# Performance work log

Hardware: AMD Instinct MI355X
Metric: run time of the kernel (lower is better)

## Reference

```python
import jax, jax.numpy as jnp
import numpy as np

N = 50000
E = 800000
F = 64
OUT = 64
K = 3


def setup_inputs() -> dict:
    key = jax.random.key(0)
    k1, k2, k3, k4, k5, k6 = jax.random.split(key, 6)
    x = jax.random.normal(k1, (N, F), dtype=jnp.float32)
    edge_row = jax.random.randint(k2, (E,), 0, N, dtype=jnp.int32)
    edge_col = jax.random.randint(k3, (E,), 0, N, dtype=jnp.int32)
    # positive edge weights (e.g., normalized adjacency values)
    edge_val = jax.random.uniform(k4, (E,), dtype=jnp.float32)
    W = jax.random.normal(k5, (F * (K + 1), OUT), dtype=jnp.float32) / np.sqrt(F * (K + 1))
    b = jax.random.normal(k6, (OUT,), dtype=jnp.float32) * 0.01
    return {"x": x, "edge_row": edge_row, "edge_col": edge_col,
            "edge_val": edge_val, "W": W, "b": b}


def _spmm(edge_row, edge_col, edge_val, h, n):
    # row i of adj @ h : sum over edges (i, j, v) of v * h[j]
    return jax.ops.segment_sum(edge_val[:, None] * h[edge_col], edge_row,
                               num_segments=n)


def reference(x, edge_row, edge_col, edge_val, W, b):
    out = x
    xs = [x]
    for _ in range(K):
        out = _spmm(edge_row, edge_col, edge_val, out, N)
        xs.append(out)
    h = jnp.concatenate(xs, axis=-1)  # [N, F*(K+1)]
    return h @ W + b
```

## Files before the change

### kernel.cpp

```cpp
#include <hip/hip_runtime.h>


#define F 64
#define OUT 64
#define SCAN_ELEMS 1024
#define NPART 8
#define CB_SHIFT 13

__global__ __launch_bounds__(256) void zero_buf(int4* __restrict__ p, int n4) {
  int i = blockIdx.x * 256 + threadIdx.x;
  if (i < n4) p[i] = make_int4(0, 0, 0, 0);
}

__global__ __launch_bounds__(256) void count_part(
    const int* __restrict__ row, const int* __restrict__ col,
    int* __restrict__ counts, int E, int rpp, int ncb) {
  int part = blockIdx.x & (NPART - 1);
  int e = (blockIdx.x >> 3) * 256 + threadIdx.x;
  if (e >= E) return;
  int r = __builtin_nontemporal_load(&row[e]);
  if ((unsigned)(r - part * rpp) >= (unsigned)rpp) return;
  int c = __builtin_nontemporal_load(&col[e]);
  atomicAdd(&counts[r * ncb + (c >> CB_SHIFT)], 1);
}

__global__ __launch_bounds__(256) void block_scan(
    const int* __restrict__ counts, int* __restrict__ offsets,
    int* __restrict__ blockSums, int B) {
  __shared__ int s[256];
  int t = threadIdx.x;
  int base = blockIdx.x * SCAN_ELEMS + t * 4;
  int v0 = 0, v1 = 0, v2 = 0, v3 = 0;
  if (base + 3 < B) {
    int4 c = *(const int4*)&counts[base];
    v0 = c.x; v1 = c.y; v2 = c.z; v3 = c.w;
  } else {
    if (base < B)     v0 = counts[base];
    if (base + 1 < B) v1 = counts[base + 1];
    if (base + 2 < B) v2 = counts[base + 2];
  }
  s[t] = v0 + v1 + v2 + v3;
  __syncthreads();
  for (int d = 1; d < 256; d <<= 1) {
    int x = (t >= d) ? s[t - d] : 0;
    __syncthreads();
    s[t] += x;
    __syncthreads();
  }
  int ex = (t == 0) ? 0 : s[t - 1];
  if (t == 255) blockSums[blockIdx.x] = s[255];
  int o0 = ex, o1 = o0 + v0, o2 = o1 + v1, o3 = o2 + v2;
  if (base + 3 < B) {
    *(int4*)&offsets[base] = make_int4(o0, o1, o2, o3);
  } else {
    if (base < B)     offsets[base]     = o0;
    if (base + 1 < B) offsets[base + 1] = o1;
    if (base + 2 < B) offsets[base + 2] = o2;
  }
}

__global__ __launch_bounds__(64) void scan_sums(int* __restrict__ bs, int nb) {
  int lane = threadIdx.x;
  int chunk = (nb + 63) / 64;
  int b = lane * chunk, e = min(b + chunk, nb);
  int sum = 0;
  for (int i = b; i < e; ++i) sum += bs[i];
  int incl = sum;
  for (int d = 1; d < 64; d <<= 1) {
    int u = __shfl_up(incl, d, 64);
    if (lane >= d) incl += u;
  }
  int run = incl - sum;
  for (int i = b; i < e; ++i) { int c = bs[i]; bs[i] = run; run += c; }
}

__global__ __launch_bounds__(256) void add_offsets(
    int* __restrict__ offsets, const int* __restrict__ blockSums,
    int* __restrict__ cursor, int B, int E) {
  int i = blockIdx.x * 256 + threadIdx.x;
  if (i < B) {
    int o = offsets[i] + blockSums[i >> 10];
    offsets[i] = o;
    cursor[i] = o;
  }
  if (i == 0) offsets[B] = E;
}

__global__ __launch_bounds__(256) void scatter_part(
    const int* __restrict__ row, const int* __restrict__ col,
    const float* __restrict__ val, int* __restrict__ cursor,
    float2* __restrict__ recs, int E, int rpp, int ncb) {
  int part = blockIdx.x & (NPART - 1);
  int e = (blockIdx.x >> 3) * 256 + threadIdx.x;
  if (e >= E) return;
  int r = __builtin_nontemporal_load(&row[e]);
  if ((unsigned)(r - part * rpp) >= (unsigned)rpp) return;
  int c = __builtin_nontemporal_load(&col[e]);
  float v = __builtin_nontemporal_load(&val[e]);
  int p = atomicAdd(&cursor[r * ncb + (c >> CB_SHIFT)], 1);
  recs[p] = make_float2(__int_as_float(c), v);
}

__global__ __launch_bounds__(256) void spmm_g16(
    const int* __restrict__ off, const float2* __restrict__ recs,
    const float* __restrict__ hin, float* __restrict__ hout, int N, int ncb) {
  int r = (blockIdx.x * 256 + threadIdx.x) >> 4;
  if (r >= N) return;
  int fp = (threadIdx.x & 15) << 2;
  int i = off[r * ncb], end = off[r * ncb + ncb];
  float4 acc = make_float4(0.f, 0.f, 0.f, 0.f);

  for (; i + 4 <= end; i += 4) {
    float2 e0 = recs[i], e1 = recs[i + 1], e2 = recs[i + 2], e3 = recs[i + 3];
    float4 h0 = *(const float4*)&hin[(size_t)__float_as_int(e0.x) * F + fp];
    float4 h1 = *(const float4*)&hin[(size_t)__float_as_int(e1.x) * F + fp];
    float4 h2 = *(const float4*)&hin[(size_t)__float_as_int(e2.x) * F + fp];
    float4 h3 = *(const float4*)&hin[(size_t)__float_as_int(e3.x) * F + fp];
    acc.x = fmaf(e0.y, h0.x, acc.x); acc.y = fmaf(e0.y, h0.y, acc.y);
    acc.z = fmaf(e0.y, h0.z, acc.z); acc.w = fmaf(e0.y, h0.w, acc.w);
    acc.x = fmaf(e1.y, h1.x, acc.x); acc.y = fmaf(e1.y, h1.y, acc.y);
    acc.z = fmaf(e1.y, h1.z, acc.z); acc.w = fmaf(e1.y, h1.w, acc.w);
    acc.x = fmaf(e2.y, h2.x, acc.x); acc.y = fmaf(e2.y, h2.y, acc.y);
    acc.z = fmaf(e2.y, h2.z, acc.z); acc.w = fmaf(e2.y, h2.w, acc.w);
    acc.x = fmaf(e3.y, h3.x, acc.x); acc.y = fmaf(e3.y, h3.y, acc.y);
    acc.z = fmaf(e3.y, h3.z, acc.z); acc.w = fmaf(e3.y, h3.w, acc.w);
  }
  for (; i < end; ++i) {
    float2 e0 = recs[i];
    float4 h0 = *(const float4*)&hin[(size_t)__float_as_int(e0.x) * F + fp];
    acc.x = fmaf(e0.y, h0.x, acc.x); acc.y = fmaf(e0.y, h0.y, acc.y);
    acc.z = fmaf(e0.y, h0.z, acc.z); acc.w = fmaf(e0.y, h0.w, acc.w);
  }
  *(float4*)&hout[(size_t)r * F + fp] = acc;
}

__global__ __launch_bounds__(256) void gemm_fused4_v5(
    const float* __restrict__ h0, const float* __restrict__ h1,
    const float* __restrict__ h2, const float* __restrict__ W,
    const float* __restrict__ bias, float* __restrict__ out, int N) {
  __shared__ float Ws[64 * 64];
  const float* hs[4] = {h0, h1, h2, out};

  int t = threadIdx.x;
  int oq = t & 3;
  int og = oq << 4;
  int ns = t >> 2;
  int node0 = blockIdx.x * 128;
  int n0 = min(node0 + ns, N - 1);
  int n1 = min(node0 + ns + 64, N - 1);

  const float4* b4 = (const float4*)bias;
  float4 acc[2][4];
#pragma unroll
  for (int m = 0; m < 4; ++m) { acc[0][m] = b4[oq * 4 + m]; acc[1][m] = acc[0][m]; }

#pragma unroll
  for (int s = 0; s < 4; ++s) {
    __syncthreads();
    const float4* Wg = (const float4*)(W + s * 4096);
#pragma unroll
    for (int i = 0; i < 4; ++i) ((float4*)Ws)[t + i * 256] = Wg[t + i * 256];
    __syncthreads();

    const float4* hr0 = (const float4*)(hs[s] + (size_t)n0 * F);
    const float4* hr1 = (const float4*)(hs[s] + (size_t)n1 * F);
    float4 hc0 = hr0[0], hc1 = hr1[0], hn0, hn1;

#pragma unroll 2
    for (int k4 = 0; k4 < 16; ++k4) {
      if (k4 < 15) { hn0 = hr0[k4 + 1]; hn1 = hr1[k4 + 1]; }
#pragma unroll
      for (int j = 0; j < 4; ++j) {
        const float4* w4 = (const float4*)&Ws[(k4 * 4 + j) * 64 + og];
        float4 w0 = w4[0], w1 = w4[1], w2 = w4[2], w3 = w4[3];
        float a = (j == 0) ? hc0.x : (j == 1) ? hc0.y : (j == 2) ? hc0.z : hc0.w;
        float c = (j == 0) ? hc1.x : (j == 1) ? hc1.y : (j == 2) ? hc1.z : hc1.w;
        acc[0][0].x = fmaf(a, w0.x, acc[0][0].x); acc[0][0].y = fmaf(a, w0.y, acc[0][0].y);
        acc[0][0].z = fmaf(a, w0.z, acc[0][0].z); acc[0][0].w = fmaf(a, w0.w, acc[0][0].w);
        acc[0][1].x = fmaf(a, w1.x, acc[0][1].x); acc[0][1].y = fmaf(a, w1.y, acc[0][1].y);
        acc[0][1].z = fmaf(a, w1.z, acc[0][1].z); acc[0][1].w = fmaf(a, w1.w, acc[0][1].w);
        acc[0][2].x = fmaf(a, w2.x, acc[0][2].x); acc[0][2].y = fmaf(a, w2.y, acc[0][2].y);
        acc[0][2].z = fmaf(a, w2.z, acc[0][2].z); acc[0][2].w = fmaf(a, w2.w, acc[0][2].w);
        acc[0][3].x = fmaf(a, w3.x, acc[0][3].x); acc[0][3].y = fmaf(a, w3.y, acc[0][3].y);
        acc[0][3].z = fmaf(a, w3.z, acc[0][3].z); acc[0][3].w = fmaf(a, w3.w, acc[0][3].w);
        acc[1][0].x = fmaf(c, w0.x, acc[1][0].x); acc[1][0].y = fmaf(c, w0.y, acc[1][0].y);
        acc[1][0].z = fmaf(c, w0.z, acc[1][0].z); acc[1][0].w = fmaf(c, w0.w, acc[1][0].w);
        acc[1][1].x = fmaf(c, w1.x, acc[1][1].x); acc[1][1].y = fmaf(c, w1.y, acc[1][1].y);
        acc[1][1].z = fmaf(c, w1.z, acc[1][1].z); acc[1][1].w = fmaf(c, w1.w, acc[1][1].w);
        acc[1][2].x = fmaf(c, w2.x, acc[1][2].x); acc[1][2].y = fmaf(c, w2.y, acc[1][2].y);
        acc[1][2].z = fmaf(c, w2.z, acc[1][2].z); acc[1][2].w = fmaf(c, w2.w, acc[1][2].w);
        acc[1][3].x = fmaf(c, w3.x, acc[1][3].x); acc[1][3].y = fmaf(c, w3.y, acc[1][3].y);
        acc[1][3].z = fmaf(c, w3.z, acc[1][3].z); acc[1][3].w = fmaf(c, w3.w, acc[1][3].w);
      }
      if (k4 < 15) { hc0 = hn0; hc1 = hn1; }
    }
  }

  int m0 = node0 + ns, m1 = node0 + ns + 64;
  if (m0 < N) {
    float4* o4 = (float4*)&out[(size_t)m0 * OUT + og];
    o4[0] = acc[0][0]; o4[1] = acc[0][1]; o4[2] = acc[0][2]; o4[3] = acc[0][3];
  }
  if (m1 < N) {
    float4* o4 = (float4*)&out[(size_t)m1 * OUT + og];
    o4[0] = acc[1][0]; o4[1] = acc[1][1]; o4[2] = acc[1][2]; o4[3] = acc[1][3];
  }
}

extern "C" void kernel_launch(void* const* d_in, const int* in_sizes, int n_in,
                              void* d_out, int out_size, void* d_ws, size_t ws_size,
                              hipStream_t stream) {
  const float* x    = (const float*)d_in[0];
  const int*   erow = (const int*)d_in[1];
  const int*   ecol = (const int*)d_in[2];
  const float* eval = (const float*)d_in[3];
  const float* W    = (const float*)d_in[4];
  const float* b    = (const float*)d_in[5];
  float* out = (float*)d_out;

  int N = in_sizes[0] / F;
  int E = in_sizes[1];
  size_t SZ = (size_t)N * F * sizeof(float);
  int ncb = ((N - 1) >> CB_SHIFT) + 1;
  int B = N * ncb;
  int nScanBlocks = (B + SCAN_ELEMS - 1) / SCAN_ELEMS;
  int rpp = (N + NPART - 1) / NPART;

  char* p = (char*)d_ws;
  float*  hA     = (float*)p;  p += SZ;
  float*  hB     = (float*)p;  p += SZ;
  float2* recs   = (float2*)p; p += (size_t)E * sizeof(float2);
  int*    counts = (int*)p;    p += (((size_t)B + 3) & ~3ull) * sizeof(int);
  int*    offs   = (int*)p;    p += (size_t)(B + 1) * sizeof(int);
  int*    cursor = (int*)p;    p += (size_t)B * sizeof(int);
  int*    bsums  = (int*)p;    p += (size_t)nScanBlocks * sizeof(int);

  int egrid = (E + 255) / 256;
  int g16grid = ((size_t)N * 16 + 255) / 256;
  int ggrid = (N + 127) / 128;
  int n4 = (B + 3) / 4;

  zero_buf<<<(n4 + 255) / 256, 256, 0, stream>>>((int4*)counts, n4);
  count_part<<<egrid * NPART, 256, 0, stream>>>(erow, ecol, counts, E, rpp, ncb);
  block_scan<<<nScanBlocks, 256, 0, stream>>>(counts, offs, bsums, B);
  scan_sums<<<1, 64, 0, stream>>>(bsums, nScanBlocks);
  add_offsets<<<(B + 255) / 256, 256, 0, stream>>>(offs, bsums, cursor, B, E);
  scatter_part<<<egrid * NPART, 256, 0, stream>>>(erow, ecol, eval, cursor, recs, E, rpp, ncb);

  spmm_g16<<<g16grid, 256, 0, stream>>>(offs, recs, x, hA, N, ncb);
  spmm_g16<<<g16grid, 256, 0, stream>>>(offs, recs, hA, hB, N, ncb);
  spmm_g16<<<g16grid, 256, 0, stream>>>(offs, recs, hB, out, N, ncb);

  gemm_fused4_v5<<<ggrid, 256, 0, stream>>>(x, hA, hB, W, b, out, N);
}
```

Baseline: 207.5 us.

## Project features through W first, then apply SpMM via Horner scheme

The four 64x64 slices of W are now applied to x up front (x·W0+b, x·W1, x·W2, x·W3), and the propagation becomes a Horner-style chain: yB += A·yC, yA += A·yB, out += A·yA. This drops the final GEMM kernel's dependency on the propagated features, so the dense projection can run in the same launch as the edge scatter. The scatter and the projection are merged into one kernel whose blocks branch on blockIdx to overlap the two. It costs one extra N×64 workspace buffer, an extra read of the addend in each SpMM, and a different floating-point summation order.

```diff
diff --git a/kernel.cpp b/kernel.cpp
--- a/kernel.cpp
+++ b/kernel.cpp
@@ -86,36 +86,113 @@
   if (i == 0) offsets[B] = E;
 }
 
-__global__ __launch_bounds__(256) void scatter_part(
+__global__ __launch_bounds__(256) void phaseB(
+    const float* __restrict__ x, const float* __restrict__ W,
+    const float* __restrict__ bias, float* __restrict__ out,
+    float* __restrict__ yA, float* __restrict__ yB, float* __restrict__ yC,
     const int* __restrict__ row, const int* __restrict__ col,
     const float* __restrict__ val, int* __restrict__ cursor,
-    float2* __restrict__ recs, int E, int rpp, int ncb) {
-  int part = blockIdx.x & (NPART - 1);
-  int e = (blockIdx.x >> 3) * 256 + threadIdx.x;
-  if (e >= E) return;
-  int r = __builtin_nontemporal_load(&row[e]);
-  if ((unsigned)(r - part * rpp) >= (unsigned)rpp) return;
-  int c = __builtin_nontemporal_load(&col[e]);
-  float v = __builtin_nontemporal_load(&val[e]);
-  int p = atomicAdd(&cursor[r * ncb + (c >> CB_SHIFT)], 1);
-  recs[p] = make_float2(__int_as_float(c), v);
-}
-
-__global__ __launch_bounds__(256) void spmm_g16(
+    float2* __restrict__ recs, int E, int rpp, int ncb, int N, int ggrid) {
+  if ((int)blockIdx.x < ggrid) {
+    __shared__ float Ws[4096];
+    float* dsts[4] = {out, yA, yB, yC};
+    int t = threadIdx.x;
+    int oq = t & 3;
+    int og = oq << 4;
+    int ns = t >> 2;
+    int node0 = blockIdx.x * 128;
+    int n0 = min(node0 + ns, N - 1);
+    int n1 = min(node0 + ns + 64, N - 1);
+    const float4* b4 = (const float4*)bias;
+    const float4* hr0 = (const float4*)(x + (size_t)n0 * F);
+    const float4* hr1 = (const float4*)(x + (size_t)n1 * F);
+
+#pragma unroll
+    for (int s = 0; s < 4; ++s) {
+      __syncthreads();
+      const float4* Wg = (const float4*)(W + s * 4096);
+#pragma unroll
+      for (int i = 0; i < 4; ++i) ((float4*)Ws)[t + i * 256] = Wg[t + i * 256];
+      __syncthreads();
+
+      float4 a0[4], a1[4];
+#pragma unroll
+      for (int m = 0; m < 4; ++m) {
+        a0[m] = (s == 0) ? b4[oq * 4 + m] : make_float4(0.f, 0.f, 0.f, 0.f);
+        a1[m] = a0[m];
+      }
+
+      float4 hc0 = hr0[0], hc1 = hr1[0], hn0, hn1;
+#pragma unroll 2
+      for (int k4 = 0; k4 < 16; ++k4) {
+        if (k4 < 15) { hn0 = hr0[k4 + 1]; hn1 = hr1[k4 + 1]; }
+#pragma unroll
+        for (int j = 0; j < 4; ++j) {
+          const float4* w4 = (const float4*)&Ws[(k4 * 4 + j) * 64 + og];
+          float4 w0 = w4[0], w1 = w4[1], w2 = w4[2], w3 = w4[3];
+          float a = (j == 0) ? hc0.x : (j == 1) ? hc0.y : (j == 2) ? hc0.z : hc0.w;
+          float c = (j == 0) ? hc1.x : (j == 1) ? hc1.y : (j == 2) ? hc1.z : hc1.w;
+          a0[0].x = fmaf(a, w0.x, a0[0].x); a0[0].y = fmaf(a, w0.y, a0[0].y);
+          a0[0].z = fmaf(a, w0.z, a0[0].z); a0[0].w = fmaf(a, w0.w, a0[0].w);
+          a0[1].x = fmaf(a, w1.x, a0[1].x); a0[1].y = fmaf(a, w1.y, a0[1].y);
+          a0[1].z = fmaf(a, w1.z, a0[1].z); a0[1].w = fmaf(a, w1.w, a0[1].w);
+          a0[2].x = fmaf(a, w2.x, a0[2].x); a0[2].y = fmaf(a, w2.y, a0[2].y);
+          a0[2].z = fmaf(a, w2.z, a0[2].z); a0[2].w = fmaf(a, w2.w, a0[2].w);
+          a0[3].x = fmaf(a, w3.x, a0[3].x); a0[3].y = fmaf(a, w3.y, a0[3].y);
+          a0[3].z = fmaf(a, w3.z, a0[3].z); a0[3].w = fmaf(a, w3.w, a0[3].w);
+          a1[0].x = fmaf(c, w0.x, a1[0].x); a1[0].y = fmaf(c, w0.y, a1[0].y);
+          a1[0].z = fmaf(c, w0.z, a1[0].z); a1[0].w = fmaf(c, w0.w, a1[0].w);
+          a1[1].x = fmaf(c, w1.x, a1[1].x); a1[1].y = fmaf(c, w1.y, a1[1].y);
+          a1[1].z = fmaf(c, w1.z, a1[1].z); a1[1].w = fmaf(c, w1.w, a1[1].w);
+          a1[2].x = fmaf(c, w2.x, a1[2].x); a1[2].y = fmaf(c, w2.y, a1[2].y);
+          a1[2].z = fmaf(c, w2.z, a1[2].z); a1[2].w = fmaf(c, w2.w, a1[2].w);
+          a1[3].x = fmaf(c, w3.x, a1[3].x); a1[3].y = fmaf(c, w3.y, a1[3].y);
+          a1[3].z = fmaf(c, w3.z, a1[3].z); a1[3].w = fmaf(c, w3.w, a1[3].w);
+        }
+        if (k4 < 15) { hc0 = hn0; hc1 = hn1; }
+      }
+
+      float* d = dsts[s];
+      int m0 = node0 + ns, m1 = node0 + ns + 64;
+      if (m0 < N) {
+        float4* o4 = (float4*)&d[(size_t)m0 * OUT + og];
+        o4[0] = a0[0]; o4[1] = a0[1]; o4[2] = a0[2]; o4[3] = a0[3];
+      }
+      if (m1 < N) {
+        float4* o4 = (float4*)&d[(size_t)m1 * OUT + og];
+        o4[0] = a1[0]; o4[1] = a1[1]; o4[2] = a1[2]; o4[3] = a1[3];
+      }
+    }
+  } else {
+    int bid = blockIdx.x - ggrid;
+    int part = bid & (NPART - 1);
+    int e = (bid >> 3) * 256 + threadIdx.x;
+    if (e >= E) return;
+    int r = __builtin_nontemporal_load(&row[e]);
+    if ((unsigned)(r - part * rpp) >= (unsigned)rpp) return;
+    int c = __builtin_nontemporal_load(&col[e]);
+    float v = __builtin_nontemporal_load(&val[e]);
+    int p = atomicAdd(&cursor[r * ncb + (c >> CB_SHIFT)], 1);
+    recs[p] = make_float2(__int_as_float(c), v);
+  }
+}
+
+__global__ __launch_bounds__(256) void spmm_add(
     const int* __restrict__ off, const float2* __restrict__ recs,
-    const float* __restrict__ hin, float* __restrict__ hout, int N, int ncb) {
+    const float* __restrict__ gsrc, const float* __restrict__ asrc,
+    float* __restrict__ dst, int N, int ncb) {
   int r = (blockIdx.x * 256 + threadIdx.x) >> 4;
   if (r >= N) return;
   int fp = (threadIdx.x & 15) << 2;
   int i = off[r * ncb], end = off[r * ncb + ncb];
-  float4 acc = make_float4(0.f, 0.f, 0.f, 0.f);
+  float4 acc = *(const float4*)&asrc[(size_t)r * F + fp];
 
   for (; i + 4 <= end; i += 4) {
     float2 e0 = recs[i], e1 = recs[i + 1], e2 = recs[i + 2], e3 = recs[i + 3];
-    float4 h0 = *(const float4*)&hin[(size_t)__float_as_int(e0.x) * F + fp];
-    float4 h1 = *(const float4*)&hin[(size_t)__float_as_int(e1.x) * F + fp];
-    float4 h2 = *(const float4*)&hin[(size_t)__float_as_int(e2.x) * F + fp];
-    float4 h3 = *(const float4*)&hin[(size_t)__float_as_int(e3.x) * F + fp];
+    float4 h0 = *(const float4*)&gsrc[(size_t)__float_as_int(e0.x) * F + fp];
+    float4 h1 = *(const float4*)&gsrc[(size_t)__float_as_int(e1.x) * F + fp];
+    float4 h2 = *(const float4*)&gsrc[(size_t)__float_as_int(e2.x) * F + fp];
+    float4 h3 = *(const float4*)&gsrc[(size_t)__float_as_int(e3.x) * F + fp];
     acc.x = fmaf(e0.y, h0.x, acc.x); acc.y = fmaf(e0.y, h0.y, acc.y);
     acc.z = fmaf(e0.y, h0.z, acc.z); acc.w = fmaf(e0.y, h0.w, acc.w);
     acc.x = fmaf(e1.y, h1.x, acc.x); acc.y = fmaf(e1.y, h1.y, acc.y);
@@ -127,84 +204,11 @@
   }
   for (; i < end; ++i) {
     float2 e0 = recs[i];
-    float4 h0 = *(const float4*)&hin[(size_t)__float_as_int(e0.x) * F + fp];
+    float4 h0 = *(const float4*)&gsrc[(size_t)__float_as_int(e0.x) * F + fp];
     acc.x = fmaf(e0.y, h0.x, acc.x); acc.y = fmaf(e0.y, h0.y, acc.y);
     acc.z = fmaf(e0.y, h0.z, acc.z); acc.w = fmaf(e0.y, h0.w, acc.w);
   }
-  *(float4*)&hout[(size_t)r * F + fp] = acc;
-}
-
-__global__ __launch_bounds__(256) void gemm_fused4_v5(
-    const float* __restrict__ h0, const float* __restrict__ h1,
-    const float* __restrict__ h2, const float* __restrict__ W,
-    const float* __restrict__ bias, float* __restrict__ out, int N) {
-  __shared__ float Ws[64 * 64];
-  const float* hs[4] = {h0, h1, h2, out};
-
-  int t = threadIdx.x;
-  int oq = t & 3;
-  int og = oq << 4;
-  int ns = t >> 2;
-  int node0 = blockIdx.x * 128;
-  int n0 = min(node0 + ns, N - 1);
-  int n1 = min(node0 + ns + 64, N - 1);
-
-  const float4* b4 = (const float4*)bias;
-  float4 acc[2][4];
-#pragma unroll
-  for (int m = 0; m < 4; ++m) { acc[0][m] = b4[oq * 4 + m]; acc[1][m] = acc[0][m]; }
-
-#pragma unroll
-  for (int s = 0; s < 4; ++s) {
-    __syncthreads();
-    const float4* Wg = (const float4*)(W + s * 4096);
-#pragma unroll
-    for (int i = 0; i < 4; ++i) ((float4*)Ws)[t + i * 256] = Wg[t + i * 256];
-    __syncthreads();
-
-    const float4* hr0 = (const float4*)(hs[s] + (size_t)n0 * F);
-    const float4* hr1 = (const float4*)(hs[s] + (size_t)n1 * F);
-    float4 hc0 = hr0[0], hc1 = hr1[0], hn0, hn1;
-
-#pragma unroll 2
-    for (int k4 = 0; k4 < 16; ++k4) {
-      if (k4 < 15) { hn0 = hr0[k4 + 1]; hn1 = hr1[k4 + 1]; }
-#pragma unroll
-      for (int j = 0; j < 4; ++j) {
-        const float4* w4 = (const float4*)&Ws[(k4 * 4 + j) * 64 + og];
-        float4 w0 = w4[0], w1 = w4[1], w2 = w4[2], w3 = w4[3];
-        float a = (j == 0) ? hc0.x : (j == 1) ? hc0.y : (j == 2) ? hc0.z : hc0.w;
-        float c = (j == 0) ? hc1.x : (j == 1) ? hc1.y : (j == 2) ? hc1.z : hc1.w;
-        acc[0][0].x = fmaf(a, w0.x, acc[0][0].x); acc[0][0].y = fmaf(a, w0.y, acc[0][0].y);
-        acc[0][0].z = fmaf(a, w0.z, acc[0][0].z); acc[0][0].w = fmaf(a, w0.w, acc[0][0].w);
-        acc[0][1].x = fmaf(a, w1.x, acc[0][1].x); acc[0][1].y = fmaf(a, w1.y, acc[0][1].y);
-        acc[0][1].z = fmaf(a, w1.z, acc[0][1].z); acc[0][1].w = fmaf(a, w1.w, acc[0][1].w);
-        acc[0][2].x = fmaf(a, w2.x, acc[0][2].x); acc[0][2].y = fmaf(a, w2.y, acc[0][2].y);
-        acc[0][2].z = fmaf(a, w2.z, acc[0][2].z); acc[0][2].w = fmaf(a, w2.w, acc[0][2].w);
-        acc[0][3].x = fmaf(a, w3.x, acc[0][3].x); acc[0][3].y = fmaf(a, w3.y, acc[0][3].y);
-        acc[0][3].z = fmaf(a, w3.z, acc[0][3].z); acc[0][3].w = fmaf(a, w3.w, acc[0][3].w);
-        acc[1][0].x = fmaf(c, w0.x, acc[1][0].x); acc[1][0].y = fmaf(c, w0.y, acc[1][0].y);
-        acc[1][0].z = fmaf(c, w0.z, acc[1][0].z); acc[1][0].w = fmaf(c, w0.w, acc[1][0].w);
-        acc[1][1].x = fmaf(c, w1.x, acc[1][1].x); acc[1][1].y = fmaf(c, w1.y, acc[1][1].y);
-        acc[1][1].z = fmaf(c, w1.z, acc[1][1].z); acc[1][1].w = fmaf(c, w1.w, acc[1][1].w);
-        acc[1][2].x = fmaf(c, w2.x, acc[1][2].x); acc[1][2].y = fmaf(c, w2.y, acc[1][2].y);
-        acc[1][2].z = fmaf(c, w2.z, acc[1][2].z); acc[1][2].w = fmaf(c, w2.w, acc[1][2].w);
-        acc[1][3].x = fmaf(c, w3.x, acc[1][3].x); acc[1][3].y = fmaf(c, w3.y, acc[1][3].y);
-        acc[1][3].z = fmaf(c, w3.z, acc[1][3].z); acc[1][3].w = fmaf(c, w3.w, acc[1][3].w);
-      }
-      if (k4 < 15) { hc0 = hn0; hc1 = hn1; }
-    }
-  }
-
-  int m0 = node0 + ns, m1 = node0 + ns + 64;
-  if (m0 < N) {
-    float4* o4 = (float4*)&out[(size_t)m0 * OUT + og];
-    o4[0] = acc[0][0]; o4[1] = acc[0][1]; o4[2] = acc[0][2]; o4[3] = acc[0][3];
-  }
-  if (m1 < N) {
-    float4* o4 = (float4*)&out[(size_t)m1 * OUT + og];
-    o4[0] = acc[1][0]; o4[1] = acc[1][1]; o4[2] = acc[1][2]; o4[3] = acc[1][3];
-  }
+  *(float4*)&dst[(size_t)r * F + fp] = acc;
 }
 
 extern "C" void kernel_launch(void* const* d_in, const int* in_sizes, int n_in,
@@ -227,8 +231,9 @@
   int rpp = (N + NPART - 1) / NPART;
 
   char* p = (char*)d_ws;
-  float*  hA     = (float*)p;  p += SZ;
-  float*  hB     = (float*)p;  p += SZ;
+  float*  yA     = (float*)p;  p += SZ;
+  float*  yB     = (float*)p;  p += SZ;
+  float*  yC     = (float*)p;  p += SZ;
   float2* recs   = (float2*)p; p += (size_t)E * sizeof(float2);
   int*    counts = (int*)p;    p += (((size_t)B + 3) & ~3ull) * sizeof(int);
   int*    offs   = (int*)p;    p += (size_t)(B + 1) * sizeof(int);
@@ -245,11 +250,12 @@
   block_scan<<<nScanBlocks, 256, 0, stream>>>(counts, offs, bsums, B);
   scan_sums<<<1, 64, 0, stream>>>(bsums, nScanBlocks);
   add_offsets<<<(B + 255) / 256, 256, 0, stream>>>(offs, bsums, cursor, B, E);
-  scatter_part<<<egrid * NPART, 256, 0, stream>>>(erow, ecol, eval, cursor, recs, E, rpp, ncb);
-
-  spmm_g16<<<g16grid, 256, 0, stream>>>(offs, recs, x, hA, N, ncb);
-  spmm_g16<<<g16grid, 256, 0, stream>>>(offs, recs, hA, hB, N, ncb);
-  spmm_g16<<<g16grid, 256, 0, stream>>>(offs, recs, hB, out, N, ncb);
-
-  gemm_fused4_v5<<<ggrid, 256, 0, stream>>>(x, hA, hB, W, b, out, N);
-}
+
+  phaseB<<<ggrid + egrid * NPART, 256, 0, stream>>>(
+      x, W, b, out, yA, yB, yC, erow, ecol, eval, cursor, recs,
+      E, rpp, ncb, N, ggrid);
+
+  spmm_add<<<g16grid, 256, 0, stream>>>(offs, recs, yC, yB, yB, N, ncb);
+  spmm_add<<<g16grid, 256, 0, stream>>>(offs, recs, yB, yA, yA, N, ncb);
+  spmm_add<<<g16grid, 256, 0, stream>>>(offs, recs, yA, out, out, N, ncb);
+}
```

New measurement: 243.4 us. 1.17x slower.

## Restructure final GEMM to stage node features in LDS and broadcast W

Applied to the files above, without the earlier changes.

The fused output GEMM is rewritten so each 512-thread block stages a 64-node tile of features in padded shared memory. Each wavefront computes 8 output columns for 64 nodes, reading W from global memory as wave-uniform broadcast loads. Results go back through shared memory so rows are stored to global memory coalesced. This trades the per-stage W copy into LDS for repeated global/L1 reads of W, and uses smaller 64-node blocks with a larger block size.

```diff
diff --git a/kernel.cpp b/kernel.cpp
--- a/kernel.cpp
+++ b/kernel.cpp
@@ -134,76 +134,65 @@
   *(float4*)&hout[(size_t)r * F + fp] = acc;
 }
 
-__global__ __launch_bounds__(256) void gemm_fused4_v5(
+__global__ __launch_bounds__(512) void gemm_ws2(
     const float* __restrict__ h0, const float* __restrict__ h1,
     const float* __restrict__ h2, const float* __restrict__ W,
     const float* __restrict__ bias, float* __restrict__ out, int N) {
-  __shared__ float Ws[64 * 64];
+  __shared__ float Hs[64 * 65];
   const float* hs[4] = {h0, h1, h2, out};
 
   int t = threadIdx.x;
-  int oq = t & 3;
-  int og = oq << 4;
-  int ns = t >> 2;
-  int node0 = blockIdx.x * 128;
-  int n0 = min(node0 + ns, N - 1);
-  int n1 = min(node0 + ns + 64, N - 1);
-
-  const float4* b4 = (const float4*)bias;
-  float4 acc[2][4];
-#pragma unroll
-  for (int m = 0; m < 4; ++m) { acc[0][m] = b4[oq * 4 + m]; acc[1][m] = acc[0][m]; }
+  int lane = t & 63;
+  int og = (t >> 6) << 3;
+  int node0 = blockIdx.x * 64;
+
+  int fr = t >> 3;
+  int fc = (t & 7) << 3;
+  int fn = min(node0 + fr, N - 1);
+
+  float a0 = bias[og + 0], a1 = bias[og + 1], a2 = bias[og + 2],
+        a3 = bias[og + 3], a4 = bias[og + 4], a5 = bias[og + 5],
+        a6 = bias[og + 6], a7 = bias[og + 7];
 
 #pragma unroll
   for (int s = 0; s < 4; ++s) {
     __syncthreads();
-    const float4* Wg = (const float4*)(W + s * 4096);
-#pragma unroll
-    for (int i = 0; i < 4; ++i) ((float4*)Ws)[t + i * 256] = Wg[t + i * 256];
-    __syncthreads();
-
-    const float4* hr0 = (const float4*)(hs[s] + (size_t)n0 * F);
-    const float4* hr1 = (const float4*)(hs[s] + (size_t)n1 * F);
-    float4 hc0 = hr0[0], hc1 = hr1[0], hn0, hn1;
-
-#pragma unroll 2
-    for (int k4 = 0; k4 < 16; ++k4) {
-      if (k4 < 15) { hn0 = hr0[k4 + 1]; hn1 = hr1[k4 + 1]; }
-#pragma unroll
-      for (int j = 0; j < 4; ++j) {
-        const float4* w4 = (const float4*)&Ws[(k4 * 4 + j) * 64 + og];
-        float4 w0 = w4[0], w1 = w4[1], w2 = w4[2], w3 = w4[3];
-        float a = (j == 0) ? hc0.x : (j == 1) ? hc0.y : (j == 2) ? hc0.z : hc0.w;
-        float c = (j == 0) ? hc1.x : (j == 1) ? hc1.y : (j == 2) ? hc1.z : hc1.w;
-        acc[0][0].x = fmaf(a, w0.x, acc[0][0].x); acc[0][0].y = fmaf(a, w0.y, acc[0][0].y);
-        acc[0][0].z = fmaf(a, w0.z, acc[0][0].z); acc[0][0].w = fmaf(a, w0.w, acc[0][0].w);
-        acc[0][1].x = fmaf(a, w1.x, acc[0][1].x); acc[0][1].y = fmaf(a, w1.y, acc[0][1].y);
-        acc[0][1].z = fmaf(a, w1.z, acc[0][1].z); acc[0][1].w = fmaf(a, w1.w, acc[0][1].w);
-        acc[0][2].x = fmaf(a, w2.x, acc[0][2].x); acc[0][2].y = fmaf(a, w2.y, acc[0][2].y);
-        acc[0][2].z = fmaf(a, w2.z, acc[0][2].z); acc[0][2].w = fmaf(a, w2.w, acc[0][2].w);
-        acc[0][3].x = fmaf(a, w3.x, acc[0][3].x); acc[0][3].y = fmaf(a, w3.y, acc[0][3].y);
-        acc[0][3].z = fmaf(a, w3.z, acc[0][3].z); acc[0][3].w = fmaf(a, w3.w, acc[0][3].w);
-        acc[1][0].x = fmaf(c, w0.x, acc[1][0].x); acc[1][0].y = fmaf(c, w0.y, acc[1][0].y);
-        acc[1][0].z = fmaf(c, w0.z, acc[1][0].z); acc[1][0].w = fmaf(c, w0.w, acc[1][0].w);
-        acc[1][1].x = fmaf(c, w1.x, acc[1][1].x); acc[1][1].y = fmaf(c, w1.y, acc[1][1].y);
-        acc[1][1].z = fmaf(c, w1.z, acc[1][1].z); acc[1][1].w = fmaf(c, w1.w, acc[1][1].w);
-        acc[1][2].x = fmaf(c, w2.x, acc[1][2].x); acc[1][2].y = fmaf(c, w2.y, acc[1][2].y);
-        acc[1][2].z = fmaf(c, w2.z, acc[1][2].z); acc[1][2].w = fmaf(c, w2.w, acc[1][2].w);
-        acc[1][3].x = fmaf(c, w3.x, acc[1][3].x); acc[1][3].y = fmaf(c, w3.y, acc[1][3].y);
-        acc[1][3].z = fmaf(c, w3.z, acc[1][3].z); acc[1][3].w = fmaf(c, w3.w, acc[1][3].w);
-      }
-      if (k4 < 15) { hc0 = hn0; hc1 = hn1; }
+    {
+      const float4* src = (const float4*)(hs[s] + (size_t)fn * F + fc);
+      float4 v0 = src[0], v1 = src[1];
+      float* d = &Hs[fr * 65 + fc];
+      d[0] = v0.x; d[1] = v0.y; d[2] = v0.z; d[3] = v0.w;
+      d[4] = v1.x; d[5] = v1.y; d[6] = v1.z; d[7] = v1.w;
     }
-  }
-
-  int m0 = node0 + ns, m1 = node0 + ns + 64;
-  if (m0 < N) {
-    float4* o4 = (float4*)&out[(size_t)m0 * OUT + og];
-    o4[0] = acc[0][0]; o4[1] = acc[0][1]; o4[2] = acc[0][2]; o4[3] = acc[0][3];
-  }
-  if (m1 < N) {
-    float4* o4 = (float4*)&out[(size_t)m1 * OUT + og];
-    o4[0] = acc[1][0]; o4[1] = acc[1][1]; o4[2] = acc[1][2]; o4[3] = acc[1][3];
+    __syncthreads();
+
+    const float* Wb = W + s * 4096 + og;
+    const float* hrow = &Hs[lane * 65];
+#pragma unroll 8
+    for (int k = 0; k < 64; ++k) {
+      float hv = hrow[k];
+      const float4* w4 = (const float4*)&Wb[k * 64];
+      float4 w0 = w4[0], w1 = w4[1];
+      a0 = fmaf(hv, w0.x, a0); a1 = fmaf(hv, w0.y, a1);
+      a2 = fmaf(hv, w0.z, a2); a3 = fmaf(hv, w0.w, a3);
+      a4 = fmaf(hv, w1.x, a4); a5 = fmaf(hv, w1.y, a5);
+      a6 = fmaf(hv, w1.z, a6); a7 = fmaf(hv, w1.w, a7);
+    }
+  }
+
+  __syncthreads();
+  {
+    float* d = &Hs[lane * 65 + og];
+    d[0] = a0; d[1] = a1; d[2] = a2; d[3] = a3;
+    d[4] = a4; d[5] = a5; d[6] = a6; d[7] = a7;
+  }
+  __syncthreads();
+  if (node0 + fr < N) {
+    const float* srow = &Hs[fr * 65 + fc];
+    float4 r0 = make_float4(srow[0], srow[1], srow[2], srow[3]);
+    float4 r1 = make_float4(srow[4], srow[5], srow[6], srow[7]);
+    float4* o4 = (float4*)&out[(size_t)(node0 + fr) * OUT + fc];
+    o4[0] = r0; o4[1] = r1;
   }
 }
 
@@ -237,7 +226,7 @@
 
   int egrid = (E + 255) / 256;
   int g16grid = ((size_t)N * 16 + 255) / 256;
-  int ggrid = (N + 127) / 128;
+  int ggrid = (N + 63) / 64;
   int n4 = (B + 3) / 4;
 
   zero_buf<<<(n4 + 255) / 256, 256, 0, stream>>>((int4*)counts, n4);
@@ -251,5 +240,5 @@
   spmm_g16<<<g16grid, 256, 0, stream>>>(offs, recs, hA, hB, N, ncb);
   spmm_g16<<<g16grid, 256, 0, stream>>>(offs, recs, hB, out, N, ncb);
 
-  gemm_fused4_v5<<<ggrid, 256, 0, stream>>>(x, hA, hB, W, b, out, N);
-}
+  gemm_ws2<<<ggrid, 512, 0, stream>>>(x, hA, hB, W, b, out, N);
+}
```

Result: slower. 296.5 us (+42.9%).
